# Performance work log

Measured on AMD Instinct MI355X. Metric: run time of the kernel, lower is better.

Reference implementation:

```python
import jax, jax.numpy as jnp
import numpy as np

B, K, P, T = 4096, 128, 64, 4

def setup_inputs() -> dict:
    key = jax.random.key(0)
    ks = jax.random.split(key, 9)
    s = lambda k, shp: jax.random.normal(k, shp, dtype=jnp.float32) * 0.1
    return {
        "x": jax.random.normal(ks[0], (B, K, 1), dtype=jnp.float32),
        "w": jax.random.normal(ks[1], (B, K, 1), dtype=jnp.float32),
        "W1": s(ks[2], (P, 1)),   # theta_1: 1 -> p
        "W2": s(ks[3], (P, P)),   # theta_2: p -> p
        "W3": s(ks[4], (P, P)),   # theta_3: p -> p
        "W4": s(ks[5], (P, 1)),   # theta_4: 1 -> p
        "W5": s(ks[6], (1, 2 * P)),  # theta_5: 2p -> 1
        "W6": s(ks[7], (P, P)),   # theta_6: p -> p
        "W7": s(ks[8], (P, P)),   # theta_7: p -> p
    }


def reference(x, w, W1, W2, W3, W4, W5, W6, W7):
    # x, w: (B, K, 1). torch Linear(in,out,bias=False): y = v @ W.T, W: (out,in)
    b, k, _ = x.shape
    p = W1.shape[0]
    # per-node feature messages (invariant across T iterations in original code)
    tmsg = jax.nn.relu(jnp.einsum('bki,pi->bkp', w, W4))   # relu(theta_4(w_k)), (B,K,p)
    sum_t = tmsg.sum(axis=1, keepdims=True)                # (B,1,p)
    xmsg = jnp.einsum('bki,pi->bkp', x, W1)                # theta_1(x_k), (B,K,p)
    mu = jnp.zeros((b, k, p), dtype=x.dtype)
    for _ in range(T):
        sum_mu = mu.sum(axis=1, keepdims=True)             # (B,1,p)
        mu = jax.nn.relu(
            xmsg
            + jnp.einsum('bkp,qp->bkq', sum_mu - mu, W2)   # theta_2(sum_mu - mu_k)
            + jnp.einsum('bkp,qp->bkq', sum_t - tmsg, W3)  # theta_3(sum_t - t_k)
        )
    pooled = jax.nn.relu(jnp.einsum('bp,qp->bq', mu.sum(axis=1), W6))  # (B,p)
    local = jnp.einsum('bkp,qp->bkq', mu, W7)                           # (B,K,p)
    # theta_5(concat(relu(theta_6(pool)), theta_7(mu_k))); split W5 = [W5a | W5b]
    W5a, W5b = W5[:, :p], W5[:, p:]
    q = jnp.einsum('bp,op->bo', pooled, W5a)[:, None, :] + jnp.einsum('bkp,op->bko', local, W5b)
    return q  # (B, K, 1)
```

## Files before the change

kernel.cpp:

```cpp
#include <hip/hip_runtime.h>

typedef __bf16 bf16;
typedef __bf16 bf16x4 __attribute__((ext_vector_type(4)));
typedef __bf16 bf16x8 __attribute__((ext_vector_type(8)));
typedef float  f32x4  __attribute__((ext_vector_type(4)));

#define MFMA16(a, b, c) __builtin_amdgcn_mfma_f32_16x16x32_bf16((a), (b), (c), 0, 0, 0)

__global__ __launch_bounds__(64, 2)
void qnet_kernel(const float* __restrict__ Xg, const float* __restrict__ Wg,
                 const float* __restrict__ W1g, const float* __restrict__ W2g,
                 const float* __restrict__ W3g, const float* __restrict__ W4g,
                 const float* __restrict__ W5g, const float* __restrict__ W6g,
                 const float* __restrict__ W7g, float* __restrict__ Outg)
{
    __shared__ __align__(16) bf16 muS[128 * 64];
    __shared__ __align__(16) float uS[64];
    __shared__ __align__(16) float smS[64];

    const int lane = threadIdx.x;
    const int b    = blockIdx.x;
    const int l15  = lane & 15;
    const int quad = lane >> 4;
    const int sw   = l15 & 7;

    float xv0 = Xg[b * 128 + lane], xv1 = Xg[b * 128 + 64 + lane];
    float wv0 = Wg[b * 128 + lane], wv1 = Wg[b * 128 + 64 + lane];

    float Ap = fmaxf(wv0, 0.f) + fmaxf(wv1, 0.f);
    float Bn = fmaxf(-wv0, 0.f) + fmaxf(-wv1, 0.f);
#pragma unroll
    for (int m = 1; m < 64; m <<= 1) { Ap += __shfl_xor(Ap, m); Bn += __shfl_xor(Bn, m); }

    float xk[8], apk[8], bnk[8];
#pragma unroll
    for (int kt = 0; kt < 8; ++kt) {
        const int src = (kt & 3) * 16 + l15;
        float xs_ = (kt < 4) ? __shfl(xv0, src) : __shfl(xv1, src);
        float ws_ = (kt < 4) ? __shfl(wv0, src) : __shfl(wv1, src);
        xk[kt]  = xs_;
        apk[kt] = Ap - fmaxf(ws_, 0.f);
        bnk[kt] = Bn - fmaxf(-ws_, 0.f);
    }

    float sp = 0.f, sm = 0.f;
#pragma unroll
    for (int c = 0; c < 16; ++c) {
        f32x4 w4 = *(const f32x4*)&W4g[c * 4];
        f32x4 w3 = *(const f32x4*)&W3g[lane * 64 + c * 4];
#pragma unroll
        for (int e = 0; e < 4; ++e) {
            sp += fmaxf(w4[e], 0.f) * w3[e];
            sm += fmaxf(-w4[e], 0.f) * w3[e];
        }
    }
    float w1C[16], v3pC[16], v3mC[16];
#pragma unroll
    for (int qt = 0; qt < 4; ++qt) {
        f32x4 w1v = *(const f32x4*)&W1g[qt * 16 + quad * 4];
#pragma unroll
        for (int e = 0; e < 4; ++e) {
            const int q = qt * 16 + quad * 4 + e;
            v3pC[qt * 4 + e] = __shfl(sp, q);
            v3mC[qt * 4 + e] = __shfl(sm, q);
            w1C[qt * 4 + e]  = w1v[e];
        }
    }

    {
        float u = 0.f;
#pragma unroll
        for (int c = 0; c < 16; ++c) {
            f32x4 w5v = *(const f32x4*)&W5g[64 + c * 4];
#pragma unroll
            for (int e = 0; e < 4; ++e) u += w5v[e] * W7g[(c * 4 + e) * 64 + lane];
        }
        uS[lane] = u;
    }

    bf16x8 w2h[4][2];
#pragma unroll
    for (int qt = 0; qt < 4; ++qt)
#pragma unroll
        for (int s = 0; s < 2; ++s) {
            const float* src = &W2g[(qt * 16 + l15) * 64 + s * 32 + quad * 8];
            f32x4 f0 = *(const f32x4*)src;
            f32x4 f1 = *(const f32x4*)(src + 4);
            bf16x8 h;
#pragma unroll
            for (int e = 0; e < 4; ++e) { h[e] = (bf16)f0[e]; h[4 + e] = (bf16)f1[e]; }
            w2h[qt][s] = h;
        }

    float smv[16];
#pragma unroll
    for (int i = 0; i < 16; ++i) smv[i] = 0.f;
#pragma unroll
    for (int kt = 0; kt < 8; ++kt) {
        const int row = (kt * 16 + l15) * 64;
#pragma unroll
        for (int qt = 0; qt < 4; ++qt) {
            bf16x4 h;
#pragma unroll
            for (int e = 0; e < 4; ++e) {
                float t = fmaf(xk[kt], w1C[qt * 4 + e],
                          fmaf(apk[kt], v3pC[qt * 4 + e], bnk[kt] * v3mC[qt * 4 + e]));
                float v = fmaxf(t, 0.f);
                smv[qt * 4 + e] += v;
                h[e] = (bf16)v;
            }
            *(bf16x4*)&muS[row + ((2 * qt + (quad >> 1)) ^ sw) * 8 + 4 * (quad & 1)] = h;
        }
    }

    const f32x4 zero4 = {0.f, 0.f, 0.f, 0.f};
    for (int it = 0; it < 3; ++it) {
#pragma unroll
        for (int m = 1; m <= 8; m <<= 1)
#pragma unroll
            for (int i = 0; i < 16; ++i) smv[i] += __shfl_xor(smv[i], m);
        if (l15 == 0) {
#pragma unroll
            for (int qt = 0; qt < 4; ++qt) {
                f32x4 v = {smv[qt * 4], smv[qt * 4 + 1], smv[qt * 4 + 2], smv[qt * 4 + 3]};
                *(f32x4*)&smS[qt * 16 + quad * 4] = v;
            }
        }
        bf16x8 bs0, bs1;
        {
            f32x4 pA = *(const f32x4*)&smS[quad * 8];
            f32x4 pB = *(const f32x4*)&smS[quad * 8 + 4];
#pragma unroll
            for (int e = 0; e < 4; ++e) {
                bf16 h = (bf16)pA[e];
                bs0[e] = (l15 == 0) ? h : ((l15 == 1) ? (bf16)(pA[e] - (float)h) : (bf16)0.f);
                bf16 g = (bf16)pB[e];
                bs0[4 + e] = (l15 == 0) ? g : ((l15 == 1) ? (bf16)(pB[e] - (float)g) : (bf16)0.f);
            }
            pA = *(const f32x4*)&smS[32 + quad * 8];
            pB = *(const f32x4*)&smS[32 + quad * 8 + 4];
#pragma unroll
            for (int e = 0; e < 4; ++e) {
                bf16 h = (bf16)pA[e];
                bs1[e] = (l15 == 0) ? h : ((l15 == 1) ? (bf16)(pA[e] - (float)h) : (bf16)0.f);
                bf16 g = (bf16)pB[e];
                bs1[4 + e] = (l15 == 0) ? g : ((l15 == 1) ? (bf16)(pB[e] - (float)g) : (bf16)0.f);
            }
        }
        f32x4 s2q[4];
#pragma unroll
        for (int qt = 0; qt < 4; ++qt) {
            f32x4 a = MFMA16(w2h[qt][0], bs0, zero4);
            a = MFMA16(w2h[qt][1], bs1, a);
#pragma unroll
            for (int e = 0; e < 4; ++e)
                s2q[qt][e] = __shfl(a[e], quad * 16) + __shfl(a[e], quad * 16 + 1);
        }

#pragma unroll
        for (int i = 0; i < 16; ++i) smv[i] = 0.f;
#pragma unroll
        for (int kt = 0; kt < 8; ++kt) {
            const int row = (kt * 16 + l15) * 64;
            bf16x8 m0 = *(const bf16x8*)&muS[row + ((quad) ^ sw) * 8];
            bf16x8 m1 = *(const bf16x8*)&muS[row + ((4 + quad) ^ sw) * 8];
#pragma unroll
            for (int qt = 0; qt < 4; ++qt) {
                f32x4 a = MFMA16(w2h[qt][0], m0, zero4);
                a = MFMA16(w2h[qt][1], m1, a);
                bf16x4 h;
#pragma unroll
                for (int e = 0; e < 4; ++e) {
                    float t = fmaf(xk[kt], w1C[qt * 4 + e], s2q[qt][e]);
                    t = fmaf(apk[kt], v3pC[qt * 4 + e], t);
                    t = fmaf(bnk[kt], v3mC[qt * 4 + e], t);
                    float v = fmaxf(t - a[e], 0.f);
                    smv[qt * 4 + e] += v;
                    h[e] = (bf16)v;
                }
                *(bf16x4*)&muS[row + ((2 * qt + (quad >> 1)) ^ sw) * 8 + 4 * (quad & 1)] = h;
            }
        }
    }

#pragma unroll
    for (int m = 1; m <= 8; m <<= 1)
#pragma unroll
        for (int i = 0; i < 16; ++i) smv[i] += __shfl_xor(smv[i], m);
    if (l15 == 0) {
#pragma unroll
        for (int qt = 0; qt < 4; ++qt) {
            f32x4 v = {smv[qt * 4], smv[qt * 4 + 1], smv[qt * 4 + 2], smv[qt * 4 + 3]};
            *(f32x4*)&smS[qt * 16 + quad * 4] = v;
        }
    }

    float pl = 0.f;
#pragma unroll
    for (int c = 0; c < 16; ++c) {
        f32x4 sv = *(const f32x4*)&smS[c * 4];
        f32x4 w6 = *(const f32x4*)&W6g[lane * 64 + c * 4];
#pragma unroll
        for (int e = 0; e < 4; ++e) pl = fmaf(sv[e], w6[e], pl);
    }
    float qa = fmaxf(pl, 0.f) * W5g[lane];
#pragma unroll
    for (int m = 1; m < 64; m <<= 1) qa += __shfl_xor(qa, m);

    f32x4 uf[2][2];
#pragma unroll
    for (int s = 0; s < 2; ++s) {
        uf[s][0] = *(const f32x4*)&uS[s * 32 + quad * 8];
        uf[s][1] = *(const f32x4*)&uS[s * 32 + quad * 8 + 4];
    }

    float res[8];
#pragma unroll
    for (int kt = 0; kt < 8; ++kt) {
        const int row = (kt * 16 + l15) * 64;
        bf16x8 m0 = *(const bf16x8*)&muS[row + ((quad) ^ sw) * 8];
        bf16x8 m1 = *(const bf16x8*)&muS[row + ((4 + quad) ^ sw) * 8];
        float r = 0.f;
#pragma unroll
        for (int j = 0; j < 4; ++j) {
            r = fmaf((float)m0[j],     uf[0][0][j], r);
            r = fmaf((float)m0[4 + j], uf[0][1][j], r);
            r = fmaf((float)m1[j],     uf[1][0][j], r);
            r = fmaf((float)m1[4 + j], uf[1][1][j], r);
        }
        r += __shfl_xor(r, 16); r += __shfl_xor(r, 32);
        res[kt] = r;
    }
    float rA0 = (quad & 1) ? res[1] : res[0];
    float rA1 = (quad & 1) ? res[3] : res[2];
    float rA  = (quad & 2) ? rA1 : rA0;
    float rB0 = (quad & 1) ? res[5] : res[4];
    float rB1 = (quad & 1) ? res[7] : res[6];
    float rB  = (quad & 2) ? rB1 : rB0;
    Outg[b * 128 + lane]      = qa + rA;
    Outg[b * 128 + 64 + lane] = qa + rB;
}

extern "C" void kernel_launch(void* const* d_in, const int* in_sizes, int n_in,
                              void* d_out, int out_size, void* d_ws, size_t ws_size,
                              hipStream_t stream) {
    (void)n_in; (void)d_ws; (void)ws_size; (void)out_size;
    const int B = in_sizes[0] >> 7;
    qnet_kernel<<<B, 64, 0, stream>>>(
        (const float*)d_in[0], (const float*)d_in[1], (const float*)d_in[2],
        (const float*)d_in[3], (const float*)d_in[4], (const float*)d_in[5],
        (const float*)d_in[6], (const float*)d_in[7], (const float*)d_in[8],
        (float*)d_out);
}
```

Baseline: 129.6 us.

## Fold per-node rank-3 affine term into MFMA with split-bf16 operands

Moves the per-element x*W1 + ap*v3p + bn*v3m computation from scalar FMAs onto an extra MFMA per tile. It packs hi/lo bf16 splits of the coefficients and node values into A/B fragments, and negates W2 so the accumulation chain yields the pre-activation directly. This removes about 48 VALU FMAs per tile and the register arrays xk/apk/bnk/w1C/v3pC/v3mC, which lowers register pressure. In exchange it adds one MFMA per tile and rebuilds the B fragment every iteration, and it may lose some precision from the truncated split products.

```diff
diff --git a/kernel.cpp b/kernel.cpp
--- a/kernel.cpp
+++ b/kernel.cpp
@@ -32,17 +32,6 @@
 #pragma unroll
     for (int m = 1; m < 64; m <<= 1) { Ap += __shfl_xor(Ap, m); Bn += __shfl_xor(Bn, m); }
 
-    float xk[8], apk[8], bnk[8];
-#pragma unroll
-    for (int kt = 0; kt < 8; ++kt) {
-        const int src = (kt & 3) * 16 + l15;
-        float xs_ = (kt < 4) ? __shfl(xv0, src) : __shfl(xv1, src);
-        float ws_ = (kt < 4) ? __shfl(wv0, src) : __shfl(wv1, src);
-        xk[kt]  = xs_;
-        apk[kt] = Ap - fmaxf(ws_, 0.f);
-        bnk[kt] = Bn - fmaxf(-ws_, 0.f);
-    }
-
     float sp = 0.f, sm = 0.f;
 #pragma unroll
     for (int c = 0; c < 16; ++c) {
@@ -54,16 +43,30 @@
             sm += fmaxf(-w4[e], 0.f) * w3[e];
         }
     }
-    float w1C[16], v3pC[16], v3mC[16];
-#pragma unroll
-    for (int qt = 0; qt < 4; ++qt) {
-        f32x4 w1v = *(const f32x4*)&W1g[qt * 16 + quad * 4];
-#pragma unroll
-        for (int e = 0; e < 4; ++e) {
-            const int q = qt * 16 + quad * 4 + e;
-            v3pC[qt * 4 + e] = __shfl(sp, q);
-            v3mC[qt * 4 + e] = __shfl(sm, q);
-            w1C[qt * 4 + e]  = w1v[e];
+
+    bf16x8 aB[4];
+    {
+        float w1l_ = W1g[lane];
+#pragma unroll
+        for (int qt = 0; qt < 4; ++qt) {
+            const int q = qt * 16 + l15;
+            float w1q = __shfl(w1l_, q);
+            float spq = __shfl(sp, q);
+            float smq = __shfl(sm, q);
+            bf16 w1h = (bf16)w1q; bf16 w1lo = (bf16)(w1q - (float)w1h);
+            bf16 vph = (bf16)spq; bf16 vplo = (bf16)(spq - (float)vph);
+            bf16 vmh = (bf16)smq; bf16 vmlo = (bf16)(smq - (float)vmh);
+            bf16x8 a;
+            const bf16 z = (bf16)0.f;
+            a[0] = (quad == 0) ? w1h  : ((quad == 1) ? vmh : z);
+            a[1] = (quad == 0) ? w1lo : z;
+            a[2] = (quad == 0) ? w1h  : z;
+            a[3] = (quad == 0) ? vph  : z;
+            a[4] = (quad == 0) ? vplo : z;
+            a[5] = (quad == 0) ? vph  : z;
+            a[6] = (quad == 0) ? vmh  : z;
+            a[7] = (quad == 0) ? vmlo : z;
+            aB[qt] = a;
         }
     }
 
@@ -78,7 +81,7 @@
         uS[lane] = u;
     }
 
-    bf16x8 w2h[4][2];
+    bf16x8 w2n[4][2];
 #pragma unroll
     for (int qt = 0; qt < 4; ++qt)
 #pragma unroll
@@ -88,24 +91,47 @@
             f32x4 f1 = *(const f32x4*)(src + 4);
             bf16x8 h;
 #pragma unroll
-            for (int e = 0; e < 4; ++e) { h[e] = (bf16)f0[e]; h[4 + e] = (bf16)f1[e]; }
-            w2h[qt][s] = h;
-        }
+            for (int e = 0; e < 4; ++e) { h[e] = (bf16)(-f0[e]); h[4 + e] = (bf16)(-f1[e]); }
+            w2n[qt][s] = h;
+        }
+
+#define BUILD_BB(bB_, kt_)                                                      \
+    {                                                                           \
+        const int src_ = ((kt_) & 3) * 16 + l15;                                \
+        float xs_ = __shfl(((kt_) < 4) ? xv0 : xv1, src_);                      \
+        float ws_ = __shfl(((kt_) < 4) ? wv0 : wv1, src_);                      \
+        float ap_ = Ap - fmaxf(ws_, 0.f);                                       \
+        float bn_ = Bn - fmaxf(-ws_, 0.f);                                      \
+        bf16 xh = (bf16)xs_; bf16 xl = (bf16)(xs_ - (float)xh);                 \
+        bf16 ah = (bf16)ap_; bf16 al = (bf16)(ap_ - (float)ah);                 \
+        bf16 bh = (bf16)bn_; bf16 bl = (bf16)(bn_ - (float)bh);                 \
+        const bf16 z_ = (bf16)0.f;                                              \
+        bB_[0] = (quad == 0) ? xh : ((quad == 1) ? bl : z_);                    \
+        bB_[1] = (quad == 0) ? xh : z_;                                         \
+        bB_[2] = (quad == 0) ? xl : z_;                                         \
+        bB_[3] = (quad == 0) ? ah : z_;                                         \
+        bB_[4] = (quad == 0) ? ah : z_;                                         \
+        bB_[5] = (quad == 0) ? al : z_;                                         \
+        bB_[6] = (quad == 0) ? bh : z_;                                         \
+        bB_[7] = (quad == 0) ? bh : z_;                                         \
+    }
+
+    const f32x4 zero4 = {0.f, 0.f, 0.f, 0.f};
 
     float smv[16];
 #pragma unroll
     for (int i = 0; i < 16; ++i) smv[i] = 0.f;
 #pragma unroll
     for (int kt = 0; kt < 8; ++kt) {
+        bf16x8 bB; BUILD_BB(bB, kt);
         const int row = (kt * 16 + l15) * 64;
 #pragma unroll
         for (int qt = 0; qt < 4; ++qt) {
+            f32x4 a = MFMA16(aB[qt], bB, zero4);
             bf16x4 h;
 #pragma unroll
             for (int e = 0; e < 4; ++e) {
-                float t = fmaf(xk[kt], w1C[qt * 4 + e],
-                          fmaf(apk[kt], v3pC[qt * 4 + e], bnk[kt] * v3mC[qt * 4 + e]));
-                float v = fmaxf(t, 0.f);
+                float v = fmaxf(a[e], 0.f);
                 smv[qt * 4 + e] += v;
                 h[e] = (bf16)v;
             }
@@ -113,7 +139,6 @@
         }
     }
 
-    const f32x4 zero4 = {0.f, 0.f, 0.f, 0.f};
     for (int it = 0; it < 3; ++it) {
 #pragma unroll
         for (int m = 1; m <= 8; m <<= 1)
@@ -150,31 +175,30 @@
         f32x4 s2q[4];
 #pragma unroll
         for (int qt = 0; qt < 4; ++qt) {
-            f32x4 a = MFMA16(w2h[qt][0], bs0, zero4);
-            a = MFMA16(w2h[qt][1], bs1, a);
+            f32x4 a = MFMA16(w2n[qt][0], bs0, zero4);
+            a = MFMA16(w2n[qt][1], bs1, a);
 #pragma unroll
             for (int e = 0; e < 4; ++e)
-                s2q[qt][e] = __shfl(a[e], quad * 16) + __shfl(a[e], quad * 16 + 1);
+                s2q[qt][e] = -(__shfl(a[e], quad * 16) + __shfl(a[e], quad * 16 + 1));
         }
 
 #pragma unroll
         for (int i = 0; i < 16; ++i) smv[i] = 0.f;
 #pragma unroll
         for (int kt = 0; kt < 8; ++kt) {
+            bf16x8 bB; BUILD_BB(bB, kt);
             const int row = (kt * 16 + l15) * 64;
             bf16x8 m0 = *(const bf16x8*)&muS[row + ((quad) ^ sw) * 8];
             bf16x8 m1 = *(const bf16x8*)&muS[row + ((4 + quad) ^ sw) * 8];
 #pragma unroll
             for (int qt = 0; qt < 4; ++qt) {
-                f32x4 a = MFMA16(w2h[qt][0], m0, zero4);
-                a = MFMA16(w2h[qt][1], m1, a);
+                f32x4 a = MFMA16(aB[qt], bB, zero4);
+                a = MFMA16(w2n[qt][0], m0, a);
+                a = MFMA16(w2n[qt][1], m1, a);
                 bf16x4 h;
 #pragma unroll
                 for (int e = 0; e < 4; ++e) {
-                    float t = fmaf(xk[kt], w1C[qt * 4 + e], s2q[qt][e]);
-                    t = fmaf(apk[kt], v3pC[qt * 4 + e], t);
-                    t = fmaf(bnk[kt], v3mC[qt * 4 + e], t);
-                    float v = fmaxf(t - a[e], 0.f);
+                    float v = fmaxf(a[e] + s2q[qt][e], 0.f);
                     smv[qt * 4 + e] += v;
                     h[e] = (bf16)v;
                 }
```

Result: slower. 143.6 us (+10.8%).
